# Kernel tuning notes

Measured on AMD Instinct MI355X. Metric: run time of the kernel, lower is better.

The kernel has to match this reference:

```python
import jax, jax.numpy as jnp
import numpy as np

V = 50000; H = 600; HH = 300; L = 100; MAX_LEN = 50; T_IN = 48; T_TGT = 50; EOS = 1


def setup_inputs() -> dict:
    key = jax.random.key(0)
    ks = iter(jax.random.split(key, 40))
    def p(shape, s=0.05):
        return jax.random.normal(next(ks), shape, dtype=jnp.float32) * s
    inp = {}
    inp["emb_enc"] = p((V, H)); inp["emb_dec"] = p((V, H))
    for pre in ["enc", "dec"]:
        for d in ["f", "b"]:
            inp[pre + "_wih_" + d] = p((3 * HH, H))
            inp[pre + "_whh_" + d] = p((3 * HH, HH))
            inp[pre + "_bih_" + d] = p((3 * HH,))
            inp[pre + "_bhh_" + d] = p((3 * HH,))
    inp["w_mean"] = p((L, H)); inp["b_mean"] = p((L,))
    inp["w_logv"] = p((L, H)); inp["b_logv"] = p((L,))
    inp["w_l2h"] = p((H, L)); inp["b_l2h"] = p((H,))
    inp["attn_w"] = p((MAX_LEN, 2 * H)); inp["attn_b"] = p((MAX_LEN,))
    inp["comb_w"] = p((H, 2 * H)); inp["comb_b"] = p((H,))
    inp["out_w"] = p((V, H)); inp["out_b"] = p((V,))
    inp["eps"] = jax.random.normal(next(ks), (MAX_LEN, L), dtype=jnp.float32)
    inp["input_tokens"] = jax.random.randint(next(ks), (T_IN,), 0, V)
    inp["target_tokens"] = jax.random.randint(next(ks), (T_TGT,), 0, V)
    return inp


def _gru_cell(x, h, wih, whh, bih, bhh):
    # PyTorch GRUCell math: r,z,n gates
    gi = wih @ x + bih
    gh = whh @ h + bhh
    ir, iz, inn = jnp.split(gi, 3)
    hr, hz, hn = jnp.split(gh, 3)
    r = jax.nn.sigmoid(ir + hr)
    zg = jax.nn.sigmoid(iz + hz)
    n = jnp.tanh(inn + r * hn)
    return (1.0 - zg) * n + zg * h


def _forward(emb_enc, emb_dec,
             enc_wih_f, enc_whh_f, enc_bih_f, enc_bhh_f,
             enc_wih_b, enc_whh_b, enc_bih_b, enc_bhh_b,
             dec_wih_f, dec_whh_f, dec_bih_f, dec_bhh_f,
             dec_wih_b, dec_whh_b, dec_bih_b, dec_bhh_b,
             w_mean, b_mean, w_logv, b_logv, w_l2h, b_l2h,
             attn_w, attn_b, comb_w, comb_b, out_w, out_b,
             eps, input_tokens, target_tokens):
    # --- encoder: bidirectional GRU fed one token at a time (both dirs see the
    # same forward stream since the original calls the GRU with seq_len=1) ---
    def enc_step(carry, tok):
        hf, hb = carry
        x = emb_enc[tok]
        hf2 = _gru_cell(x, hf, enc_wih_f, enc_whh_f, enc_bih_f, enc_bhh_f)
        hb2 = _gru_cell(x, hb, enc_wih_b, enc_whh_b, enc_bih_b, enc_bhh_b)
        return (hf2, hb2), jnp.concatenate([hf2, hb2])
    h0 = jnp.zeros((HH,), dtype=emb_enc.dtype)
    (hf, hb), enc_out = jax.lax.scan(enc_step, (h0, h0), input_tokens)
    enc_outputs = jnp.zeros((MAX_LEN, H), dtype=emb_enc.dtype).at[:input_tokens.shape[0]].set(enc_out)
    # --- latent ---
    mean = enc_outputs @ w_mean.T + b_mean          # (MAX_LEN, L)
    logv = enc_outputs @ w_logv.T + b_logv          # (MAX_LEN, L)
    z = eps * jnp.exp(0.5 * logv) + mean
    latent_out = z @ w_l2h.T + b_l2h                # (MAX_LEN, H)
    # --- decoder with attention over latent_out (teacher forcing) ---
    dec_in = jnp.concatenate([jnp.array([EOS], dtype=target_tokens.dtype), target_tokens[:-1]])
    def dec_step(carry, tok):
        hf, hb = carry
        emb = emb_dec[tok]                          # (H,) dropout==identity (eval)
        hflat = jnp.concatenate([hf, hb])           # (H,)
        aw = jax.nn.softmax(attn_w @ jnp.concatenate([emb, hflat]) + attn_b)  # (MAX_LEN,)
        applied = aw @ latent_out                   # (H,)
        o = jax.nn.relu(comb_w @ jnp.concatenate([emb, applied]) + comb_b)
        hf2 = _gru_cell(o, hf, dec_wih_f, dec_whh_f, dec_bih_f, dec_bhh_f)
        hb2 = _gru_cell(o, hb, dec_wih_b, dec_whh_b, dec_bih_b, dec_bhh_b)
        logp = jax.nn.log_softmax(out_w @ jnp.concatenate([hf2, hb2]) + out_b)
        return (hf2, hb2), logp
    _, decoded = jax.lax.scan(dec_step, (hf, hb), dec_in)  # (T_TGT, V)
    return decoded, mean, logv


def reference(emb_enc, emb_dec,
              enc_wih_f, enc_whh_f, enc_bih_f, enc_bhh_f,
              enc_wih_b, enc_whh_b, enc_bih_b, enc_bhh_b,
              dec_wih_f, dec_whh_f, dec_bih_f, dec_bhh_f,
              dec_wih_b, dec_whh_b, dec_bih_b, dec_bhh_b,
              w_mean, b_mean, w_logv, b_logv, w_l2h, b_l2h,
              attn_w, attn_b, comb_w, comb_b, out_w, out_b,
              eps, input_tokens, target_tokens):
    return _forward(emb_enc, emb_dec,
                    enc_wih_f, enc_whh_f, enc_bih_f, enc_bhh_f,
                    enc_wih_b, enc_whh_b, enc_bih_b, enc_bhh_b,
                    dec_wih_f, dec_whh_f, dec_bih_f, dec_bhh_f,
                    dec_wih_b, dec_whh_b, dec_bih_b, dec_bhh_b,
                    w_mean, b_mean, w_logv, b_logv, w_l2h, b_l2h,
                    attn_w, attn_b, comb_w, comb_b, out_w, out_b,
                    eps, input_tokens, target_tokens)
```

## Files before the change

### kernel.cpp

```cpp
#include <hip/hip_runtime.h>
#include <math.h>

#define VSZ 50000
#define HD 600
#define HHD 300
#define LATD 100
#define MLEN 50
#define TIN 48
#define TTGT 50
#define NBLK 75
#define NTHR 512
#define NTOT (NBLK*NTHR)
#define ESTR 640
#define SLOT_STRIDE 32
#define SENTU 0x40000000u

typedef __attribute__((ext_vector_type(4))) float f32x4;
typedef __attribute__((ext_vector_type(8))) short s16x8;

__device__ __forceinline__ float sigf(float x){ return 1.0f/(1.0f+__expf(-x)); }

__device__ __forceinline__ void stf(float* p, float v){
    __hip_atomic_store((unsigned int*)p, __float_as_uint(v),
                       __ATOMIC_RELAXED, __HIP_MEMORY_SCOPE_AGENT);
}
__device__ __forceinline__ void stu(float* p, unsigned v){
    __hip_atomic_store((unsigned int*)p, v,
                       __ATOMIC_RELAXED, __HIP_MEMORY_SCOPE_AGENT);
}
__device__ __forceinline__ int ldslot(const int* p){
    return __hip_atomic_load(p, __ATOMIC_RELAXED, __HIP_MEMORY_SCOPE_AGENT);
}
__device__ __forceinline__ void stslot(int* p, int v){
    __hip_atomic_store(p, v, __ATOMIC_RELAXED, __HIP_MEMORY_SCOPE_AGENT);
}

__device__ __forceinline__ f32x4 ld_unc16(const float* p){
    f32x4 r;
    asm volatile("global_load_dwordx4 %0, %1, off sc0 sc1\n\ts_waitcnt vmcnt(0)"
                 : "=v"(r) : "v"(p) : "memory");
    return r;
}
__device__ __forceinline__ f32x4 poll16(const float* p){
    f32x4 r = ld_unc16(p);
    while (__float_as_uint(r[0])==SENTU || __float_as_uint(r[1])==SENTU ||
           __float_as_uint(r[2])==SENTU || __float_as_uint(r[3])==SENTU){
        __builtin_amdgcn_s_sleep(1);
        r = ld_unc16(p);
    }
    return r;
}

__device__ __forceinline__ void redu3(float&a,float&b,float&c){
    #pragma unroll
    for(int off=32;off;off>>=1){
        a+=__shfl_xor(a,off); b+=__shfl_xor(b,off); c+=__shfl_xor(c,off);
    }
}
__device__ __forceinline__ void redu6(float&a,float&b,float&c,float&d,float&e,float&f){
    #pragma unroll
    for(int off=32;off;off>>=1){
        a+=__shfl_xor(a,off); b+=__shfl_xor(b,off); c+=__shfl_xor(c,off);
        d+=__shfl_xor(d,off); e+=__shfl_xor(e,off); f+=__shfl_xor(f,off);
    }
}

__device__ __forceinline__ void gridbar(int* slots, int* flags, int e){
    asm volatile("s_waitcnt vmcnt(0)" ::: "memory");
    __syncthreads();
    const int tid = threadIdx.x;
    if (tid == 0) stslot(&slots[blockIdx.x*SLOT_STRIDE], e);
    if (blockIdx.x == 0){
        if (tid < NBLK){
            while (ldslot(&slots[tid*SLOT_STRIDE]) < e)
                __builtin_amdgcn_s_sleep(1);
        }
        __syncthreads();
        if (tid < NBLK) stslot(&flags[tid*SLOT_STRIDE], e);
    } else {
        if (tid == 0){
            while (ldslot(&flags[blockIdx.x*SLOT_STRIDE]) < e)
                __builtin_amdgcn_s_sleep(1);
        }
    }
    __syncthreads();
}

__global__ void k_init(int* sync_mem){
    int i = blockIdx.x*blockDim.x + threadIdx.x;
    if (i < 2*NBLK*SLOT_STRIDE) sync_mem[i] = 0;
}

__global__ void __launch_bounds__(NTHR) k_seq(
    const float* __restrict__ emb_enc, const float* __restrict__ emb_dec,
    const float* __restrict__ enc_wih_f, const float* __restrict__ enc_whh_f,
    const float* __restrict__ enc_bih_f, const float* __restrict__ enc_bhh_f,
    const float* __restrict__ enc_wih_b, const float* __restrict__ enc_whh_b,
    const float* __restrict__ enc_bih_b, const float* __restrict__ enc_bhh_b,
    const float* __restrict__ dec_wih_f, const float* __restrict__ dec_whh_f,
    const float* __restrict__ dec_bih_f, const float* __restrict__ dec_bhh_f,
    const float* __restrict__ dec_wih_b, const float* __restrict__ dec_whh_b,
    const float* __restrict__ dec_bih_b, const float* __restrict__ dec_bhh_b,
    const float* __restrict__ w_mean, const float* __restrict__ b_mean,
    const float* __restrict__ w_logv, const float* __restrict__ b_logv,
    const float* __restrict__ w_l2h, const float* __restrict__ b_l2h,
    const float* __restrict__ attn_w, const float* __restrict__ attn_b,
    const float* __restrict__ comb_w, const float* __restrict__ comb_b,
    const float* __restrict__ eps, const int* __restrict__ in_toks,
    const int* __restrict__ tgt_toks,
    float* __restrict__ GIf, float* __restrict__ ENCf,
    float* __restrict__ Zf, float* __restrict__ LATf, float* __restrict__ Mf,
    float* __restrict__ APREf, float* __restrict__ CPREf,
    float* __restrict__ HSs, float* __restrict__ HSv,
    float* __restrict__ out_mean, float* __restrict__ out_logv,
    int* slots, int* flags){

    __shared__ float h_lds[ESTR];
    __shared__ float o_lds[ESTR];
    __shared__ float s_lds[64];
    __shared__ float aw_lds[64];
    __shared__ float hv_lds[8];
    __shared__ float big_lds[HD*MLEN];

    const int tid  = threadIdx.x;
    const int lane = tid & 63;
    const int wid  = tid >> 6;
    const int gtid = blockIdx.x*NTHR + tid;
    const int gw   = blockIdx.x*8 + wid;
    const int dir  = gw / HHD;
    const int k    = gw % HHD;
    int ep = 0;

    if (tid < ESTR-HD){ h_lds[HD+tid]=0.f; o_lds[HD+tid]=0.f; }

    for (int idx=gtid; idx<TIN*HD; idx+=NTOT){
        int t=idx/HD, j=idx%HD;
        stu(&ENCf[(long)t*ESTR + j], SENTU);
    }
    for (int idx=gtid; idx<TTGT*HD; idx+=NTOT){
        int t=idx/HD, j=idx%HD;
        stu(&HSs[(long)t*ESTR + j], SENTU);
    }
    for (int idx=gtid; idx<TIN*1800; idx+=NTOT){
        int t=idx/1800, r=idx%1800, d=r/900, j=r%900;
        const float* w  = d ? enc_wih_b : enc_wih_f;
        const float* bi = d ? enc_bih_b : enc_bih_f;
        const float* x  = emb_enc + (long)in_toks[t]*HD;
        const float* wr = w + (long)j*HD;
        float acc = bi[j];
        for (int kk=0;kk<HD;kk+=4){
            float4 wv = *(const float4*)(wr+kk);
            float4 xv = *(const float4*)(x+kk);
            acc = fmaf(wv.x,xv.x,acc); acc = fmaf(wv.y,xv.y,acc);
            acc = fmaf(wv.z,xv.z,acc); acc = fmaf(wv.w,xv.w,acc);
        }
        stf(&GIf[idx], acc);
    }
    for (int idx=gtid; idx<TTGT*MLEN; idx+=NTOT){
        int t=idx/MLEN, a=idx%MLEN;
        int tok = t ? tgt_toks[t-1] : 1;
        const float* x  = emb_dec + (long)tok*HD;
        const float* wr = attn_w + (long)a*1200;
        float acc = attn_b[a];
        for (int kk=0;kk<HD;kk+=4){
            float4 wv = *(const float4*)(wr+kk);
            float4 xv = *(const float4*)(x+kk);
            acc = fmaf(wv.x,xv.x,acc); acc = fmaf(wv.y,xv.y,acc);
            acc = fmaf(wv.z,xv.z,acc); acc = fmaf(wv.w,xv.w,acc);
        }
        stf(&APREf[idx], acc);
    }
    for (int idx=gtid; idx<TTGT*HD; idx+=NTOT){
        int t=idx/HD, j=idx%HD;
        int tok = t ? tgt_toks[t-1] : 1;
        const float* x  = emb_dec + (long)tok*HD;
        const float* wr = comb_w + (long)j*1200;
        float acc = comb_b[j];
        for (int kk=0;kk<HD;kk+=4){
            float4 wv = *(const float4*)(wr+kk);
            float4 xv = *(const float4*)(x+kk);
            acc = fmaf(wv.x,xv.x,acc); acc = fmaf(wv.y,xv.y,acc);
            acc = fmaf(wv.z,xv.z,acc); acc = fmaf(wv.w,xv.w,acc);
        }
        stf(&CPREf[idx], acc);
    }
    gridbar(slots, flags, ++ep);

    {
        const float* whh = dir ? enc_whh_b : enc_whh_f;
        const float* bhh = dir ? enc_bhh_b : enc_bhh_f;
        float wr_[5], wz_[5], wn_[5];
        #pragma unroll
        for (int i=0;i<5;i++){
            int k2 = lane + 64*i;
            bool ok = k2 < HHD;
            wr_[i] = ok ? whh[(long)k*HHD + k2] : 0.f;
            wz_[i] = ok ? whh[(long)(HHD+k)*HHD + k2] : 0.f;
            wn_[i] = ok ? whh[(long)(2*HHD+k)*HHD + k2] : 0.f;
        }
        const float bhr = bhh[k], bhz = bhh[HHD+k], bhn = bhh[2*HHD+k];
        float gr=0, gz=0, gn=0;
        if (lane < TIN){
            const float* g = GIf + (long)lane*1800 + dir*900;
            gr = g[k]; gz = g[HHD+k]; gn = g[2*HHD+k];
        }
        for (int t=0; t<TIN; t++){
            if (t){
                if (tid < HD/4)
                    *(f32x4*)&h_lds[4*tid] = poll16(&ENCf[(long)(t-1)*ESTR + 4*tid]);
            } else {
                h_lds[tid] = 0.f;
                if (tid < HD-NTHR) h_lds[NTHR+tid] = 0.f;
            }
            __syncthreads();
            if (t){
                big_lds[(long)(t-1)*HD + tid] = h_lds[tid];
                if (tid < HD-NTHR) big_lds[(long)(t-1)*HD + NTHR + tid] = h_lds[NTHR+tid];
            }
            float sr=0, sz=0, sn=0;
            #pragma unroll
            for (int i=0;i<5;i++){
                float hv = h_lds[dir*HHD + lane + 64*i];
                sr = fmaf(wr_[i], hv, sr);
                sz = fmaf(wz_[i], hv, sz);
                sn = fmaf(wn_[i], hv, sn);
            }
            redu3(sr, sz, sn);
            float grt=__shfl(gr,t), gzt=__shfl(gz,t), gnt=__shfl(gn,t);
            if (lane==0){
                float r = sigf(grt + sr + bhr);
                float z = sigf(gzt + sz + bhz);
                float n = tanhf(gnt + r*(sn + bhn));
                float hp = h_lds[gw];
                hv_lds[wid] = (1.f-z)*n + z*hp;
            }
            __syncthreads();
            if (tid < 8) stf(&ENCf[(long)t*ESTR + blockIdx.x*8 + tid], hv_lds[tid]);
        }
        if (tid < HD/4)
            *(f32x4*)&h_lds[4*tid] = poll16(&ENCf[(long)(TIN-1)*ESTR + 4*tid]);
        __syncthreads();
        big_lds[(long)(TIN-1)*HD + tid] = h_lds[tid];
        if (tid < HD-NTHR) big_lds[(long)(TIN-1)*HD + NTHR + tid] = h_lds[NTHR+tid];
        big_lds[TIN*HD + tid] = 0.f;
        big_lds[TIN*HD + NTHR + tid] = 0.f;
        if (tid < 2*HD - 2*NTHR) big_lds[TIN*HD + 2*NTHR + tid] = 0.f;
        __syncthreads();
    }

    for (int idx=gtid; idx<MLEN*LATD; idx+=NTOT){
        int i=idx/LATD, l=idx%LATD;
        const float* e = &big_lds[(long)i*HD];
        const float* wmr = w_mean + (long)l*HD;
        float am = b_mean[l];
        for (int kk=0;kk<HD;kk+=4){
            f32x4 wv = *(const f32x4*)(wmr+kk);
            f32x4 ev = *(const f32x4*)(e+kk);
            am = fmaf(wv[0],ev[0],am); am = fmaf(wv[1],ev[1],am);
            am = fmaf(wv[2],ev[2],am); am = fmaf(wv[3],ev[3],am);
        }
        const float* wlr = w_logv + (long)l*HD;
        float al = b_logv[l];
        for (int kk=0;kk<HD;kk+=4){
            f32x4 wv = *(const f32x4*)(wlr+kk);
            f32x4 ev = *(const f32x4*)(e+kk);
            al = fmaf(wv[0],ev[0],al); al = fmaf(wv[1],ev[1],al);
            al = fmaf(wv[2],ev[2],al); al = fmaf(wv[3],ev[3],al);
        }
        out_mean[idx] = am;
        out_logv[idx] = al;
        stf(&Zf[idx], eps[idx]*__expf(0.5f*al) + am);
    }
    gridbar(slots, flags, ++ep);
    for (int idx=gtid; idx<MLEN*HD; idx+=NTOT){
        int i=idx/HD, j=idx%HD;
        const float* zr = Zf + (long)i*LATD;
        const float* wr = w_l2h + (long)j*LATD;
        float acc = b_l2h[j];
        for (int kk=0;kk<LATD;kk+=4){
            float4 wv = *(const float4*)(wr+kk);
            float4 zv = *(const float4*)(zr+kk);
            acc = fmaf(wv.x,zv.x,acc); acc = fmaf(wv.y,zv.y,acc);
            acc = fmaf(wv.z,zv.z,acc); acc = fmaf(wv.w,zv.w,acc);
        }
        stf(&LATf[idx], acc);
    }
    gridbar(slots, flags, ++ep);
    for (int idx=gtid; idx<MLEN*HD; idx+=NTOT){
        int j=idx/MLEN, i=idx%MLEN;
        const float* wr = comb_w + (long)j*1200 + HD;
        const float* lr = LATf + (long)i*HD;
        float acc = 0.f;
        for (int kk=0;kk<HD;kk+=4){
            float4 wv = *(const float4*)(wr+kk);
            float4 lv = *(const float4*)(lr+kk);
            acc = fmaf(wv.x,lv.x,acc); acc = fmaf(wv.y,lv.y,acc);
            acc = fmaf(wv.z,lv.z,acc); acc = fmaf(wv.w,lv.w,acc);
        }
        stf(&Mf[idx], acc);
    }
    gridbar(slots, flags, ++ep);

    {
        for (int idx=tid; idx<HD*MLEN/4; idx+=NTHR)
            *(f32x4*)&big_lds[4*idx] = *(const f32x4*)&Mf[4*idx];

        const float* wih = dir ? dec_wih_b : dec_wih_f;
        const float* bih = dir ? dec_bih_b : dec_bih_f;
        const float* whh = dir ? dec_whh_b : dec_whh_f;
        const float* bhh = dir ? dec_bhh_b : dec_bhh_f;
        float ur[10], uz[10], un[10];
        #pragma unroll
        for (int i=0;i<10;i++){
            int k2 = lane + 64*i;
            bool ok = k2 < HD;
            ur[i] = ok ? wih[(long)k*HD + k2] : 0.f;
            uz[i] = ok ? wih[(long)(HHD+k)*HD + k2] : 0.f;
            un[i] = ok ? wih[(long)(2*HHD+k)*HD + k2] : 0.f;
        }
        float vr[5], vz[5], vn[5];
        #pragma unroll
        for (int i=0;i<5;i++){
            int k2 = lane + 64*i;
            bool ok = k2 < HHD;
            vr[i] = ok ? whh[(long)k*HHD + k2] : 0.f;
            vz[i] = ok ? whh[(long)(HHD+k)*HHD + k2] : 0.f;
            vn[i] = ok ? whh[(long)(2*HHD+k)*HHD + k2] : 0.f;
        }
        const float bir = bih[k], biz = bih[HHD+k], bin_ = bih[2*HHD+k];
        const float bhr = bhh[k], bhz = bhh[HHD+k], bhn = bhh[2*HHD+k];

        for (int t=0; t<TTGT; t++){
            if (t){
                if (tid < HD/4)
                    *(f32x4*)&h_lds[4*tid] = poll16(&HSs[(long)(t-1)*ESTR + 4*tid]);
            }
            float cp0 = CPREf[(long)t*HD + tid];
            float cp1 = (tid < HD-NTHR) ? CPREf[(long)t*HD + NTHR + tid] : 0.f;
            __syncthreads();
            for (int a=wid; a<MLEN; a+=8){
                const float* arow = attn_w + (long)a*1200 + HD;
                float acc = 0.f;
                #pragma unroll
                for (int i=0;i<10;i++){
                    int kk = lane + 64*i;
                    if (kk < HD) acc = fmaf(arow[kk], h_lds[kk], acc);
                }
                #pragma unroll
                for (int off=32;off;off>>=1) acc += __shfl_xor(acc,off);
                if (lane==0) s_lds[a] = acc + APREf[t*MLEN + a];
            }
            __syncthreads();
            if (tid==0){
                float m = -1e30f;
                for (int a=0;a<MLEN;a++) m = fmaxf(m, s_lds[a]);
                float sum = 0.f;
                for (int a=0;a<MLEN;a++){ float e = __expf(s_lds[a]-m); aw_lds[a]=e; sum+=e; }
                float inv = 1.f/sum;
                for (int a=0;a<MLEN;a++) aw_lds[a] *= inv;
            }
            __syncthreads();
            {
                float acc = cp0;
                const float* mr = &big_lds[tid*MLEN];
                #pragma unroll
                for (int i=0;i<MLEN;i++) acc = fmaf(mr[i], aw_lds[i], acc);
                o_lds[tid] = fmaxf(acc, 0.f);
                if (tid < HD-NTHR){
                    float acc2 = cp1;
                    const float* mr2 = &big_lds[(NTHR+tid)*MLEN];
                    #pragma unroll
                    for (int i=0;i<MLEN;i++) acc2 = fmaf(mr2[i], aw_lds[i], acc2);
                    o_lds[NTHR+tid] = fmaxf(acc2, 0.f);
                }
            }
            __syncthreads();
            float ar=0,az=0,an=0, hr=0,hz=0,hn=0;
            #pragma unroll
            for (int i=0;i<10;i++){
                float ov = o_lds[lane + 64*i];
                ar = fmaf(ur[i], ov, ar);
                az = fmaf(uz[i], ov, az);
                an = fmaf(un[i], ov, an);
            }
            #pragma unroll
            for (int i=0;i<5;i++){
                float hv = h_lds[dir*HHD + lane + 64*i];
                hr = fmaf(vr[i], hv, hr);
                hz = fmaf(vz[i], hv, hz);
                hn = fmaf(vn[i], hv, hn);
            }
            redu6(ar,az,an,hr,hz,hn);
            if (lane==0){
                float r = sigf(ar + bir + hr + bhr);
                float zg = sigf(az + biz + hz + bhz);
                float n = tanhf(an + bin_ + r*(hn + bhn));
                hv_lds[wid] = (1.f-zg)*n + zg*h_lds[gw];
            }
            __syncthreads();
            if (tid < 8){
                float hnew = hv_lds[tid];
                stf(&HSs[(long)t*ESTR + blockIdx.x*8 + tid], hnew);
                HSv[(long)t*HD + blockIdx.x*8 + tid] = hnew;
            }
        }
    }
}

__device__ __forceinline__ s16x8 pack8(const float* __restrict__ p){
    s16x8 r;
    #pragma unroll
    for (int i=0;i<8;i++){
        unsigned u = __float_as_uint(p[i]);
        r[i] = (short)((u + 0x7fffu + ((u>>16)&1u)) >> 16);
    }
    return r;
}

__global__ void __launch_bounds__(256) k_vocab(const float* __restrict__ out_w,
        const float* __restrict__ out_b, const float* __restrict__ HS,
        float* __restrict__ logits){
    int lane = threadIdx.x & 63, wid = threadIdx.x >> 6;
    int vbase = blockIdx.x*64 + wid*16;
    int arow  = vbase + (lane & 15);
    int kg    = (lane >> 4) * 8;
    bool aok  = arow < VSZ;
    const float* ap = out_w + (long)(aok ? arow : 0) * HD;
    int t0 = lane & 15;
    f32x4 acc0 = {0,0,0,0}, acc1 = acc0, acc2 = acc0, acc3 = acc0;
    const s16x8 zf = (s16x8)0;

    for (int ks=0; ks<19; ks++){
        int kb = ks*32 + kg;
        bool kok = kb < HD;
        s16x8 a = (aok && kok) ? pack8(ap + kb) : zf;
        s16x8 b0 = kok              ? pack8(HS + (long)(t0     )*HD + kb) : zf;
        s16x8 b1 = kok              ? pack8(HS + (long)(t0 + 16)*HD + kb) : zf;
        s16x8 b2 = kok              ? pack8(HS + (long)(t0 + 32)*HD + kb) : zf;
        s16x8 b3 = (kok && t0 < 2)  ? pack8(HS + (long)(t0 + 48)*HD + kb) : zf;
        acc0 = __builtin_amdgcn_mfma_f32_16x16x32_bf16(a, b0, acc0, 0,0,0);
        acc1 = __builtin_amdgcn_mfma_f32_16x16x32_bf16(a, b1, acc1, 0,0,0);
        acc2 = __builtin_amdgcn_mfma_f32_16x16x32_bf16(a, b2, acc2, 0,0,0);
        acc3 = __builtin_amdgcn_mfma_f32_16x16x32_bf16(a, b3, acc3, 0,0,0);
    }

    int vst = vbase + (lane>>4)*4;
    float bb[4];
    #pragma unroll
    for (int r=0;r<4;r++) bb[r] = (vst+r < VSZ) ? out_b[vst+r] : 0.f;
    #pragma unroll
    for (int f=0; f<4; f++){
        int t = t0 + 16*f;
        if (t >= TTGT) continue;
        const f32x4 acc = f==0?acc0 : f==1?acc1 : f==2?acc2 : acc3;
        float* rowp = logits + (long)t*VSZ;
        #pragma unroll
        for (int r=0;r<4;r++){
            int v = vst + r;
            if (v < VSZ) rowp[v] = acc[r] + bb[r];
        }
    }
}

__global__ void __launch_bounds__(1024) k_lsm(float* __restrict__ logits){
    __shared__ float red[16];
    __shared__ float sm, sl;
    long t = blockIdx.x;
    float* row = logits + t*VSZ;
    int tid = threadIdx.x, lane = tid&63, w = tid>>6;
    float m = -1e30f;
    for (int v=tid; v<VSZ; v+=1024) m = fmaxf(m, row[v]);
    #pragma unroll
    for (int off=32;off;off>>=1) m = fmaxf(m, __shfl_xor(m,off));
    if (lane==0) red[w] = m;
    __syncthreads();
    if (tid==0){ float mm=red[0]; for (int i=1;i<16;i++) mm=fmaxf(mm,red[i]); sm=mm; }
    __syncthreads();
    float mx = sm;
    float s = 0.f;
    for (int v=tid; v<VSZ; v+=1024) s += __expf(row[v]-mx);
    #pragma unroll
    for (int off=32;off;off>>=1) s += __shfl_xor(s,off);
    __syncthreads();
    if (lane==0) red[w] = s;
    __syncthreads();
    if (tid==0){ float ss=0.f; for (int i=0;i<16;i++) ss+=red[i]; sl = logf(ss); }
    __syncthreads();
    float lg = sl;
    for (int v=tid; v<VSZ; v+=1024) row[v] = row[v] - mx - lg;
}

extern "C" void kernel_launch(void* const* d_in, const int* in_sizes, int n_in,
                              void* d_out, int out_size, void* d_ws, size_t ws_size,
                              hipStream_t stream) {
    const float* emb_enc   = (const float*)d_in[0];
    const float* emb_dec   = (const float*)d_in[1];
    const float* enc_wih_f = (const float*)d_in[2];
    const float* enc_whh_f = (const float*)d_in[3];
    const float* enc_bih_f = (const float*)d_in[4];
    const float* enc_bhh_f = (const float*)d_in[5];
    const float* enc_wih_b = (const float*)d_in[6];
    const float* enc_whh_b = (const float*)d_in[7];
    const float* enc_bih_b = (const float*)d_in[8];
    const float* enc_bhh_b = (const float*)d_in[9];
    const float* dec_wih_f = (const float*)d_in[10];
    const float* dec_whh_f = (const float*)d_in[11];
    const float* dec_bih_f = (const float*)d_in[12];
    const float* dec_bhh_f = (const float*)d_in[13];
    const float* dec_wih_b = (const float*)d_in[14];
    const float* dec_whh_b = (const float*)d_in[15];
    const float* dec_bih_b = (const float*)d_in[16];
    const float* dec_bhh_b = (const float*)d_in[17];
    const float* w_mean    = (const float*)d_in[18];
    const float* b_mean    = (const float*)d_in[19];
    const float* w_logv    = (const float*)d_in[20];
    const float* b_logv    = (const float*)d_in[21];
    const float* w_l2h     = (const float*)d_in[22];
    const float* b_l2h     = (const float*)d_in[23];
    const float* attn_w    = (const float*)d_in[24];
    const float* attn_b    = (const float*)d_in[25];
    const float* comb_w    = (const float*)d_in[26];
    const float* comb_b    = (const float*)d_in[27];
    const float* out_w     = (const float*)d_in[28];
    const float* out_b     = (const float*)d_in[29];
    const float* eps       = (const float*)d_in[30];
    const int*   in_toks   = (const int*)d_in[31];
    const int*   tgt_toks  = (const int*)d_in[32];

    float* ws = (float*)d_ws;
    float* GIf   = ws;
    float* ENCf  = ws + 86400;
    float* Zf    = ws + 118400;
    float* LATf  = ws + 123424;
    float* Mf    = ws + 153440;
    float* APREf = ws + 183456;
    float* CPREf = ws + 185984;
    float* HSs   = ws + 216000;
    float* HSv   = ws + 248000;
    int*   slots = (int*)(ws + 278016);
    int*   flags = (int*)(ws + 280416);

    float* dec_out  = (float*)d_out;
    float* out_mean = dec_out + 2500000;
    float* out_logv = dec_out + 2505000;

    k_init<<<(2*NBLK*SLOT_STRIDE + 255)/256, 256, 0, stream>>>((int*)(ws + 278016));

    k_seq<<<NBLK, NTHR, 0, stream>>>(
        emb_enc, emb_dec,
        enc_wih_f, enc_whh_f, enc_bih_f, enc_bhh_f,
        enc_wih_b, enc_whh_b, enc_bih_b, enc_bhh_b,
        dec_wih_f, dec_whh_f, dec_bih_f, dec_bhh_f,
        dec_wih_b, dec_whh_b, dec_bih_b, dec_bhh_b,
        w_mean, b_mean, w_logv, b_logv, w_l2h, b_l2h,
        attn_w, attn_b, comb_w, comb_b,
        eps, in_toks, tgt_toks,
        GIf, ENCf, Zf, LATf, Mf, APREf, CPREf, HSs, HSv,
        out_mean, out_logv, slots, flags);

    k_vocab<<<(VSZ + 63)/64, 256, 0, stream>>>(out_w, out_b, HSv, dec_out);
    k_lsm<<<TTGT, 1024, 0, stream>>>(dec_out);
}
```

Baseline: 850.2 us.

## Shrink persistent recurrent grid to 10 blocks with four hidden units per wave

The persistent sequential kernel drops from 75×512 to 10×1024 threads, and each wave now computes four GRU hidden units whose weights stay in registers. Per-step results are written with uncached 16-byte stores. The embedding and input projections plus sentinel initialisation move to a separate wide pre-kernel, which removes the first grid barrier. Attention weights are also cached in registers for the decoder. Fewer blocks should make the per-step cross-block polling cheaper, at the cost of much higher register pressure and less parallelism per step.

```diff
diff --git a/kernel.cpp b/kernel.cpp
--- a/kernel.cpp
+++ b/kernel.cpp
@@ -8,8 +8,8 @@
 #define MLEN 50
 #define TIN 48
 #define TTGT 50
-#define NBLK 75
-#define NTHR 512
+#define NBLK 10
+#define NTHR 1024
 #define NTOT (NBLK*NTHR)
 #define ESTR 640
 #define SLOT_STRIDE 32
@@ -22,10 +22,6 @@
 
 __device__ __forceinline__ void stf(float* p, float v){
     __hip_atomic_store((unsigned int*)p, __float_as_uint(v),
-                       __ATOMIC_RELAXED, __HIP_MEMORY_SCOPE_AGENT);
-}
-__device__ __forceinline__ void stu(float* p, unsigned v){
-    __hip_atomic_store((unsigned int*)p, v,
                        __ATOMIC_RELAXED, __HIP_MEMORY_SCOPE_AGENT);
 }
 __device__ __forceinline__ int ldslot(const int* p){
@@ -40,6 +36,10 @@
     asm volatile("global_load_dwordx4 %0, %1, off sc0 sc1\n\ts_waitcnt vmcnt(0)"
                  : "=v"(r) : "v"(p) : "memory");
     return r;
+}
+__device__ __forceinline__ void st_unc16(float* p, f32x4 v){
+    asm volatile("global_store_dwordx4 %0, %1, off sc0 sc1"
+                 :: "v"(p), "v"(v) : "memory");
 }
 __device__ __forceinline__ f32x4 poll16(const float* p){
     f32x4 r = ld_unc16(p);
@@ -88,60 +88,26 @@
 
 __global__ void k_init(int* sync_mem){
     int i = blockIdx.x*blockDim.x + threadIdx.x;
-    if (i < 2*NBLK*SLOT_STRIDE) sync_mem[i] = 0;
-}
-
-__global__ void __launch_bounds__(NTHR) k_seq(
+    if (i < 2*64*SLOT_STRIDE) sync_mem[i] = 0;
+}
+
+__global__ void __launch_bounds__(512) k_pre(
     const float* __restrict__ emb_enc, const float* __restrict__ emb_dec,
-    const float* __restrict__ enc_wih_f, const float* __restrict__ enc_whh_f,
-    const float* __restrict__ enc_bih_f, const float* __restrict__ enc_bhh_f,
-    const float* __restrict__ enc_wih_b, const float* __restrict__ enc_whh_b,
-    const float* __restrict__ enc_bih_b, const float* __restrict__ enc_bhh_b,
-    const float* __restrict__ dec_wih_f, const float* __restrict__ dec_whh_f,
-    const float* __restrict__ dec_bih_f, const float* __restrict__ dec_bhh_f,
-    const float* __restrict__ dec_wih_b, const float* __restrict__ dec_whh_b,
-    const float* __restrict__ dec_bih_b, const float* __restrict__ dec_bhh_b,
-    const float* __restrict__ w_mean, const float* __restrict__ b_mean,
-    const float* __restrict__ w_logv, const float* __restrict__ b_logv,
-    const float* __restrict__ w_l2h, const float* __restrict__ b_l2h,
+    const float* __restrict__ enc_wih_f, const float* __restrict__ enc_bih_f,
+    const float* __restrict__ enc_wih_b, const float* __restrict__ enc_bih_b,
     const float* __restrict__ attn_w, const float* __restrict__ attn_b,
     const float* __restrict__ comb_w, const float* __restrict__ comb_b,
-    const float* __restrict__ eps, const int* __restrict__ in_toks,
-    const int* __restrict__ tgt_toks,
-    float* __restrict__ GIf, float* __restrict__ ENCf,
-    float* __restrict__ Zf, float* __restrict__ LATf, float* __restrict__ Mf,
-    float* __restrict__ APREf, float* __restrict__ CPREf,
-    float* __restrict__ HSs, float* __restrict__ HSv,
-    float* __restrict__ out_mean, float* __restrict__ out_logv,
-    int* slots, int* flags){
-
-    __shared__ float h_lds[ESTR];
-    __shared__ float o_lds[ESTR];
-    __shared__ float s_lds[64];
-    __shared__ float aw_lds[64];
-    __shared__ float hv_lds[8];
-    __shared__ float big_lds[HD*MLEN];
-
-    const int tid  = threadIdx.x;
-    const int lane = tid & 63;
-    const int wid  = tid >> 6;
-    const int gtid = blockIdx.x*NTHR + tid;
-    const int gw   = blockIdx.x*8 + wid;
-    const int dir  = gw / HHD;
-    const int k    = gw % HHD;
-    int ep = 0;
-
-    if (tid < ESTR-HD){ h_lds[HD+tid]=0.f; o_lds[HD+tid]=0.f; }
-
-    for (int idx=gtid; idx<TIN*HD; idx+=NTOT){
-        int t=idx/HD, j=idx%HD;
-        stu(&ENCf[(long)t*ESTR + j], SENTU);
-    }
-    for (int idx=gtid; idx<TTGT*HD; idx+=NTOT){
-        int t=idx/HD, j=idx%HD;
-        stu(&HSs[(long)t*ESTR + j], SENTU);
-    }
-    for (int idx=gtid; idx<TIN*1800; idx+=NTOT){
+    const int* __restrict__ in_toks, const int* __restrict__ tgt_toks,
+    float* __restrict__ GIf, float* __restrict__ APREf, float* __restrict__ CPREf,
+    float* __restrict__ ENCf, float* __restrict__ HSs){
+    const int g  = blockIdx.x*512 + threadIdx.x;
+    const int NT = gridDim.x*512;
+    const float SENT = __uint_as_float(SENTU);
+    for (int idx=g; idx<TIN*HD; idx+=NT)
+        ENCf[(long)(idx/HD)*ESTR + idx%HD] = SENT;
+    for (int idx=g; idx<TTGT*HD; idx+=NT)
+        HSs[(long)(idx/HD)*ESTR + idx%HD] = SENT;
+    for (int idx=g; idx<TIN*1800; idx+=NT){
         int t=idx/1800, r=idx%1800, d=r/900, j=r%900;
         const float* w  = d ? enc_wih_b : enc_wih_f;
         const float* bi = d ? enc_bih_b : enc_bih_f;
@@ -154,9 +120,9 @@
             acc = fmaf(wv.x,xv.x,acc); acc = fmaf(wv.y,xv.y,acc);
             acc = fmaf(wv.z,xv.z,acc); acc = fmaf(wv.w,xv.w,acc);
         }
-        stf(&GIf[idx], acc);
-    }
-    for (int idx=gtid; idx<TTGT*MLEN; idx+=NTOT){
+        GIf[idx] = acc;
+    }
+    for (int idx=g; idx<TTGT*MLEN; idx+=NT){
         int t=idx/MLEN, a=idx%MLEN;
         int tok = t ? tgt_toks[t-1] : 1;
         const float* x  = emb_dec + (long)tok*HD;
@@ -168,9 +134,9 @@
             acc = fmaf(wv.x,xv.x,acc); acc = fmaf(wv.y,xv.y,acc);
             acc = fmaf(wv.z,xv.z,acc); acc = fmaf(wv.w,xv.w,acc);
         }
-        stf(&APREf[idx], acc);
-    }
-    for (int idx=gtid; idx<TTGT*HD; idx+=NTOT){
+        APREf[idx] = acc;
+    }
+    for (int idx=g; idx<TTGT*HD; idx+=NT){
         int t=idx/HD, j=idx%HD;
         int tok = t ? tgt_toks[t-1] : 1;
         const float* x  = emb_dec + (long)tok*HD;
@@ -182,69 +148,115 @@
             acc = fmaf(wv.x,xv.x,acc); acc = fmaf(wv.y,xv.y,acc);
             acc = fmaf(wv.z,xv.z,acc); acc = fmaf(wv.w,xv.w,acc);
         }
-        stf(&CPREf[idx], acc);
-    }
-    gridbar(slots, flags, ++ep);
+        CPREf[idx] = acc;
+    }
+}
+
+__global__ void __launch_bounds__(NTHR) k_seq(
+    const float* __restrict__ enc_whh_f, const float* __restrict__ enc_bhh_f,
+    const float* __restrict__ enc_whh_b, const float* __restrict__ enc_bhh_b,
+    const float* __restrict__ dec_wih_f, const float* __restrict__ dec_whh_f,
+    const float* __restrict__ dec_bih_f, const float* __restrict__ dec_bhh_f,
+    const float* __restrict__ dec_wih_b, const float* __restrict__ dec_whh_b,
+    const float* __restrict__ dec_bih_b, const float* __restrict__ dec_bhh_b,
+    const float* __restrict__ w_mean, const float* __restrict__ b_mean,
+    const float* __restrict__ w_logv, const float* __restrict__ b_logv,
+    const float* __restrict__ w_l2h, const float* __restrict__ b_l2h,
+    const float* __restrict__ attn_w, const float* __restrict__ comb_w,
+    const float* __restrict__ eps,
+    const float* __restrict__ GIf, float* __restrict__ ENCf,
+    float* __restrict__ Zf, float* __restrict__ LATf, float* __restrict__ Mf,
+    const float* __restrict__ APREf, const float* __restrict__ CPREf,
+    float* __restrict__ HSs, float* __restrict__ HSv,
+    float* __restrict__ out_mean, float* __restrict__ out_logv,
+    int* slots, int* flags){
+
+    __shared__ float h_lds[ESTR];
+    __shared__ float o_lds[ESTR];
+    __shared__ float s_lds[64];
+    __shared__ float aw_lds[64];
+    __shared__ float big_lds[HD*MLEN];
+
+    const int tid  = threadIdx.x;
+    const int lane = tid & 63;
+    const int wid  = tid >> 6;
+    const int gtid = blockIdx.x*NTHR + tid;
+    const int W    = blockIdx.x*16 + wid;
+    const bool act = W < 150;
+    const int Wc   = act ? W : 0;
+    const int dir  = (Wc*4) / HHD;
+    const int kb   = Wc*4 - dir*HHD;
+    int ep = 0;
+
+    if (tid < ESTR-HD){ h_lds[HD+tid]=0.f; o_lds[HD+tid]=0.f; }
 
     {
         const float* whh = dir ? enc_whh_b : enc_whh_f;
         const float* bhh = dir ? enc_bhh_b : enc_bhh_f;
-        float wr_[5], wz_[5], wn_[5];
+        float wr_[4][5], wz_[4][5], wn_[4][5];
+        float bhr_[4], bhz_[4], bhn_[4];
         #pragma unroll
-        for (int i=0;i<5;i++){
-            int k2 = lane + 64*i;
-            bool ok = k2 < HHD;
-            wr_[i] = ok ? whh[(long)k*HHD + k2] : 0.f;
-            wz_[i] = ok ? whh[(long)(HHD+k)*HHD + k2] : 0.f;
-            wn_[i] = ok ? whh[(long)(2*HHD+k)*HHD + k2] : 0.f;
-        }
-        const float bhr = bhh[k], bhz = bhh[HHD+k], bhn = bhh[2*HHD+k];
-        float gr=0, gz=0, gn=0;
-        if (lane < TIN){
-            const float* g = GIf + (long)lane*1800 + dir*900;
-            gr = g[k]; gz = g[HHD+k]; gn = g[2*HHD+k];
+        for (int q=0;q<4;q++){
+            int kq = kb + q;
+            #pragma unroll
+            for (int i=0;i<5;i++){
+                int k2 = lane + 64*i;
+                bool ok = k2 < HHD;
+                wr_[q][i] = ok ? whh[(long)kq*HHD + k2] : 0.f;
+                wz_[q][i] = ok ? whh[(long)(HHD+kq)*HHD + k2] : 0.f;
+                wn_[q][i] = ok ? whh[(long)(2*HHD+kq)*HHD + k2] : 0.f;
+            }
+            bhr_[q] = bhh[kq]; bhz_[q] = bhh[HHD+kq]; bhn_[q] = bhh[2*HHD+kq];
+        }
+        float gr_[4], gz_[4], gn_[4];
+        #pragma unroll
+        for (int q=0;q<4;q++){
+            if (lane < TIN){
+                const float* g = GIf + (long)lane*1800 + dir*900 + kb + q;
+                gr_[q] = g[0]; gz_[q] = g[HHD]; gn_[q] = g[2*HHD];
+            } else { gr_[q]=0.f; gz_[q]=0.f; gn_[q]=0.f; }
         }
         for (int t=0; t<TIN; t++){
             if (t){
                 if (tid < HD/4)
                     *(f32x4*)&h_lds[4*tid] = poll16(&ENCf[(long)(t-1)*ESTR + 4*tid]);
             } else {
-                h_lds[tid] = 0.f;
-                if (tid < HD-NTHR) h_lds[NTHR+tid] = 0.f;
-            }
-            __syncthreads();
-            if (t){
-                big_lds[(long)(t-1)*HD + tid] = h_lds[tid];
-                if (tid < HD-NTHR) big_lds[(long)(t-1)*HD + NTHR + tid] = h_lds[NTHR+tid];
-            }
-            float sr=0, sz=0, sn=0;
-            #pragma unroll
-            for (int i=0;i<5;i++){
-                float hv = h_lds[dir*HHD + lane + 64*i];
-                sr = fmaf(wr_[i], hv, sr);
-                sz = fmaf(wz_[i], hv, sz);
-                sn = fmaf(wn_[i], hv, sn);
-            }
-            redu3(sr, sz, sn);
-            float grt=__shfl(gr,t), gzt=__shfl(gz,t), gnt=__shfl(gn,t);
-            if (lane==0){
-                float r = sigf(grt + sr + bhr);
-                float z = sigf(gzt + sz + bhz);
-                float n = tanhf(gnt + r*(sn + bhn));
-                float hp = h_lds[gw];
-                hv_lds[wid] = (1.f-z)*n + z*hp;
-            }
-            __syncthreads();
-            if (tid < 8) stf(&ENCf[(long)t*ESTR + blockIdx.x*8 + tid], hv_lds[tid]);
+                if (tid < HD) h_lds[tid] = 0.f;
+            }
+            __syncthreads();
+            if (t && tid < HD) big_lds[(long)(t-1)*HD + tid] = h_lds[tid];
+            float hnew[4];
+            #pragma unroll
+            for (int q=0;q<4;q++){
+                float sr=0, sz=0, sn=0;
+                #pragma unroll
+                for (int i=0;i<5;i++){
+                    float hv = h_lds[dir*HHD + lane + 64*i];
+                    sr = fmaf(wr_[q][i], hv, sr);
+                    sz = fmaf(wz_[q][i], hv, sz);
+                    sn = fmaf(wn_[q][i], hv, sn);
+                }
+                redu3(sr, sz, sn);
+                float grt=__shfl(gr_[q],t), gzt=__shfl(gz_[q],t), gnt=__shfl(gn_[q],t);
+                float r = sigf(grt + sr + bhr_[q]);
+                float z = sigf(gzt + sz + bhz_[q]);
+                float n = tanhf(gnt + r*(sn + bhn_[q]));
+                hnew[q] = (1.f-z)*n + z*h_lds[dir*HHD + kb + q];
+            }
+            if (act && lane==0){
+                f32x4 v = {hnew[0], hnew[1], hnew[2], hnew[3]};
+                st_unc16(&ENCf[(long)t*ESTR + W*4], v);
+            }
+            __syncthreads();
         }
         if (tid < HD/4)
             *(f32x4*)&h_lds[4*tid] = poll16(&ENCf[(long)(TIN-1)*ESTR + 4*tid]);
         __syncthreads();
-        big_lds[(long)(TIN-1)*HD + tid] = h_lds[tid];
-        if (tid < HD-NTHR) big_lds[(long)(TIN-1)*HD + NTHR + tid] = h_lds[NTHR+tid];
-        big_lds[TIN*HD + tid] = 0.f;
-        big_lds[TIN*HD + NTHR + tid] = 0.f;
-        if (tid < 2*HD - 2*NTHR) big_lds[TIN*HD + 2*NTHR + tid] = 0.f;
+        if (tid < HD){
+            big_lds[(long)(TIN-1)*HD + tid] = h_lds[tid];
+            big_lds[(long)TIN*HD + tid] = 0.f;
+            big_lds[(long)(TIN+1)*HD + tid] = 0.f;
+        }
         __syncthreads();
     }
 
@@ -305,50 +317,65 @@
         for (int idx=tid; idx<HD*MLEN/4; idx+=NTHR)
             *(f32x4*)&big_lds[4*idx] = *(const f32x4*)&Mf[4*idx];
 
+        float aw_[4][10];
+        #pragma unroll
+        for (int ai=0;ai<4;ai++){
+            int a = wid + 16*ai;
+            #pragma unroll
+            for (int i=0;i<10;i++){
+                int kk = lane + 64*i;
+                aw_[ai][i] = (a < MLEN && kk < HD) ? attn_w[(long)a*1200 + HD + kk] : 0.f;
+            }
+        }
         const float* wih = dir ? dec_wih_b : dec_wih_f;
         const float* bih = dir ? dec_bih_b : dec_bih_f;
         const float* whh = dir ? dec_whh_b : dec_whh_f;
         const float* bhh = dir ? dec_bhh_b : dec_bhh_f;
-        float ur[10], uz[10], un[10];
+        float ur_[4][10], uz_[4][10], un_[4][10];
+        float vr_[4][5], vz_[4][5], vn_[4][5];
+        float bir_[4], biz_[4], bin_[4], bhr_[4], bhz_[4], bhn_[4];
         #pragma unroll
-        for (int i=0;i<10;i++){
-            int k2 = lane + 64*i;
-            bool ok = k2 < HD;
-            ur[i] = ok ? wih[(long)k*HD + k2] : 0.f;
-            uz[i] = ok ? wih[(long)(HHD+k)*HD + k2] : 0.f;
-            un[i] = ok ? wih[(long)(2*HHD+k)*HD + k2] : 0.f;
-        }
-        float vr[5], vz[5], vn[5];
-        #pragma unroll
-        for (int i=0;i<5;i++){
-            int k2 = lane + 64*i;
-            bool ok = k2 < HHD;
-            vr[i] = ok ? whh[(long)k*HHD + k2] : 0.f;
-            vz[i] = ok ? whh[(long)(HHD+k)*HHD + k2] : 0.f;
-            vn[i] = ok ? whh[(long)(2*HHD+k)*HHD + k2] : 0.f;
-        }
-        const float bir = bih[k], biz = bih[HHD+k], bin_ = bih[2*HHD+k];
-        const float bhr = bhh[k], bhz = bhh[HHD+k], bhn = bhh[2*HHD+k];
+        for (int q=0;q<4;q++){
+            int kq = kb + q;
+            #pragma unroll
+            for (int i=0;i<10;i++){
+                int k2 = lane + 64*i;
+                bool ok = k2 < HD;
+                ur_[q][i] = ok ? wih[(long)kq*HD + k2] : 0.f;
+                uz_[q][i] = ok ? wih[(long)(HHD+kq)*HD + k2] : 0.f;
+                un_[q][i] = ok ? wih[(long)(2*HHD+kq)*HD + k2] : 0.f;
+            }
+            #pragma unroll
+            for (int i=0;i<5;i++){
+                int k2 = lane + 64*i;
+                bool ok = k2 < HHD;
+                vr_[q][i] = ok ? whh[(long)kq*HHD + k2] : 0.f;
+                vz_[q][i] = ok ? whh[(long)(HHD+kq)*HHD + k2] : 0.f;
+                vn_[q][i] = ok ? whh[(long)(2*HHD+kq)*HHD + k2] : 0.f;
+            }
+            bir_[q] = bih[kq]; biz_[q] = bih[HHD+kq]; bin_[q] = bih[2*HHD+kq];
+            bhr_[q] = bhh[kq]; bhz_[q] = bhh[HHD+kq]; bhn_[q] = bhh[2*HHD+kq];
+        }
 
         for (int t=0; t<TTGT; t++){
             if (t){
                 if (tid < HD/4)
                     *(f32x4*)&h_lds[4*tid] = poll16(&HSs[(long)(t-1)*ESTR + 4*tid]);
             }
-            float cp0 = CPREf[(long)t*HD + tid];
-            float cp1 = (tid < HD-NTHR) ? CPREf[(long)t*HD + NTHR + tid] : 0.f;
-            __syncthreads();
-            for (int a=wid; a<MLEN; a+=8){
-                const float* arow = attn_w + (long)a*1200 + HD;
-                float acc = 0.f;
-                #pragma unroll
-                for (int i=0;i<10;i++){
-                    int kk = lane + 64*i;
-                    if (kk < HD) acc = fmaf(arow[kk], h_lds[kk], acc);
+            float cp = (tid < HD) ? CPREf[(long)t*HD + tid] : 0.f;
+            __syncthreads();
+            #pragma unroll
+            for (int ai=0;ai<4;ai++){
+                int a = wid + 16*ai;
+                if (a < MLEN){
+                    float acc = 0.f;
+                    #pragma unroll
+                    for (int i=0;i<10;i++)
+                        acc = fmaf(aw_[ai][i], h_lds[lane + 64*i], acc);
+                    #pragma unroll
+                    for (int off=32;off;off>>=1) acc += __shfl_xor(acc,off);
+                    if (lane==0) s_lds[a] = acc + APREf[t*MLEN + a];
                 }
-                #pragma unroll
-                for (int off=32;off;off>>=1) acc += __shfl_xor(acc,off);
-                if (lane==0) s_lds[a] = acc + APREf[t*MLEN + a];
             }
             __syncthreads();
             if (tid==0){
@@ -360,49 +387,44 @@
                 for (int a=0;a<MLEN;a++) aw_lds[a] *= inv;
             }
             __syncthreads();
-            {
-                float acc = cp0;
+            if (tid < HD){
+                float acc = cp;
                 const float* mr = &big_lds[tid*MLEN];
                 #pragma unroll
                 for (int i=0;i<MLEN;i++) acc = fmaf(mr[i], aw_lds[i], acc);
                 o_lds[tid] = fmaxf(acc, 0.f);
-                if (tid < HD-NTHR){
-                    float acc2 = cp1;
-                    const float* mr2 = &big_lds[(NTHR+tid)*MLEN];
-                    #pragma unroll
-                    for (int i=0;i<MLEN;i++) acc2 = fmaf(mr2[i], aw_lds[i], acc2);
-                    o_lds[NTHR+tid] = fmaxf(acc2, 0.f);
+            }
+            __syncthreads();
+            float hnew[4];
+            #pragma unroll
+            for (int q=0;q<4;q++){
+                float ar=0,az=0,an=0, hr=0,hz=0,hn=0;
+                #pragma unroll
+                for (int i=0;i<10;i++){
+                    float ov = o_lds[lane + 64*i];
+                    ar = fmaf(ur_[q][i], ov, ar);
+                    az = fmaf(uz_[q][i], ov, az);
+                    an = fmaf(un_[q][i], ov, an);
                 }
-            }
-            __syncthreads();
-            float ar=0,az=0,an=0, hr=0,hz=0,hn=0;
-            #pragma unroll
-            for (int i=0;i<10;i++){
-                float ov = o_lds[lane + 64*i];
-                ar = fmaf(ur[i], ov, ar);
-                az = fmaf(uz[i], ov, az);
-                an = fmaf(un[i], ov, an);
-            }
-            #pragma unroll
-            for (int i=0;i<5;i++){
-                float hv = h_lds[dir*HHD + lane + 64*i];
-                hr = fmaf(vr[i], hv, hr);
-                hz = fmaf(vz[i], hv, hz);
-                hn = fmaf(vn[i], hv, hn);
-            }
-            redu6(ar,az,an,hr,hz,hn);
-            if (lane==0){
-                float r = sigf(ar + bir + hr + bhr);
-                float zg = sigf(az + biz + hz + bhz);
-                float n = tanhf(an + bin_ + r*(hn + bhn));
-                hv_lds[wid] = (1.f-zg)*n + zg*h_lds[gw];
-            }
-            __syncthreads();
-            if (tid < 8){
-                float hnew = hv_lds[tid];
-                stf(&HSs[(long)t*ESTR + blockIdx.x*8 + tid], hnew);
-                HSv[(long)t*HD + blockIdx.x*8 + tid] = hnew;
-            }
+                #pragma unroll
+                for (int i=0;i<5;i++){
+                    float hv = h_lds[dir*HHD + lane + 64*i];
+                    hr = fmaf(vr_[q][i], hv, hr);
+                    hz = fmaf(vz_[q][i], hv, hz);
+                    hn = fmaf(vn_[q][i], hv, hn);
+                }
+                redu6(ar,az,an,hr,hz,hn);
+                float r = sigf(ar + bir_[q] + hr + bhr_[q]);
+                float zg = sigf(az + biz_[q] + hz + bhz_[q]);
+                float n = tanhf(an + bin_[q] + r*(hn + bhn_[q]));
+                hnew[q] = (1.f-zg)*n + zg*h_lds[dir*HHD + kb + q];
+            }
+            if (act && lane==0){
+                f32x4 v = {hnew[0], hnew[1], hnew[2], hnew[3]};
+                st_unc16(&HSs[(long)t*ESTR + W*4], v);
+                *(f32x4*)&HSv[(long)t*HD + W*4] = v;
+            }
+            __syncthreads();
         }
     }
 }
@@ -538,23 +560,27 @@
     float* HSs   = ws + 216000;
     float* HSv   = ws + 248000;
     int*   slots = (int*)(ws + 278016);
-    int*   flags = (int*)(ws + 280416);
+    int*   flags = (int*)(ws + 280064);
 
     float* dec_out  = (float*)d_out;
     float* out_mean = dec_out + 2500000;
     float* out_logv = dec_out + 2505000;
 
-    k_init<<<(2*NBLK*SLOT_STRIDE + 255)/256, 256, 0, stream>>>((int*)(ws + 278016));
+    k_init<<<(2*64*SLOT_STRIDE + 255)/256, 256, 0, stream>>>((int*)(ws + 278016));
+
+    k_pre<<<150, 512, 0, stream>>>(
+        emb_enc, emb_dec,
+        enc_wih_f, enc_bih_f, enc_wih_b, enc_bih_b,
+        attn_w, attn_b, comb_w, comb_b,
+        in_toks, tgt_toks,
+        GIf, APREf, CPREf, ENCf, HSs);
 
     k_seq<<<NBLK, NTHR, 0, stream>>>(
-        emb_enc, emb_dec,
-        enc_wih_f, enc_whh_f, enc_bih_f, enc_bhh_f,
-        enc_wih_b, enc_whh_b, enc_bih_b, enc_bhh_b,
+        enc_whh_f, enc_bhh_f, enc_whh_b, enc_bhh_b,
         dec_wih_f, dec_whh_f, dec_bih_f, dec_bhh_f,
         dec_wih_b, dec_whh_b, dec_bih_b, dec_bhh_b,
         w_mean, b_mean, w_logv, b_logv, w_l2h, b_l2h,
-        attn_w, attn_b, comb_w, comb_b,
-        eps, in_toks, tgt_toks,
+        attn_w, comb_w, eps,
         GIf, ENCf, Zf, LATf, Mf, APREf, CPREf, HSs, HSv,
         out_mean, out_logv, slots, flags);
 
```

Result: slower. 2.172 ms (+155.5%).

## Poll only own-direction encoder state per step and cache attention weights in registers

Applied to the files above, without the earlier changes.

In the encoder loop each block now polls only the half of the hidden state its direction needs, rather than the full vector. The other half is gathered once after the loop to fill the encoder outputs buffer. The decoder preloads its attention-weight rows into registers and replaces the single-thread softmax with a wave-level shuffle reduction. Launch bounds are changed to request two blocks per CU. Together these aim to shorten the per-step latency on the serial critical path, at the cost of much higher register pressure from the 70-float awr array plus the existing weight registers, which risks spilling.

```diff
diff --git a/kernel.cpp b/kernel.cpp
--- a/kernel.cpp
+++ b/kernel.cpp
@@ -91,7 +91,7 @@
     if (i < 2*NBLK*SLOT_STRIDE) sync_mem[i] = 0;
 }
 
-__global__ void __launch_bounds__(NTHR) k_seq(
+__global__ void __launch_bounds__(NTHR, 2) k_seq(
     const float* __restrict__ emb_enc, const float* __restrict__ emb_dec,
     const float* __restrict__ enc_wih_f, const float* __restrict__ enc_whh_f,
     const float* __restrict__ enc_bih_f, const float* __restrict__ enc_bhh_f,
@@ -131,7 +131,12 @@
     const int k    = gw % HHD;
     int ep = 0;
 
-    if (tid < ESTR-HD){ h_lds[HD+tid]=0.f; o_lds[HD+tid]=0.f; }
+    const int dlo = (blockIdx.x*8) / HHD, dhi = (blockIdx.x*8 + 7) / HHD;
+    const int clo = (dlo==dhi) ? dlo*75 : 0;
+    const int chi = (dlo==dhi) ? clo+75 : 150;
+    const int flo = 4*clo, fhi = 4*chi;
+
+    for (int j=tid; j<ESTR; j+=NTHR){ h_lds[j]=0.f; o_lds[j]=0.f; }
 
     for (int idx=gtid; idx<TIN*HD; idx+=NTOT){
         int t=idx/HD, j=idx%HD;
@@ -206,16 +211,13 @@
         }
         for (int t=0; t<TIN; t++){
             if (t){
-                if (tid < HD/4)
-                    *(f32x4*)&h_lds[4*tid] = poll16(&ENCf[(long)(t-1)*ESTR + 4*tid]);
-            } else {
-                h_lds[tid] = 0.f;
-                if (tid < HD-NTHR) h_lds[NTHR+tid] = 0.f;
+                if (tid < chi-clo)
+                    *(f32x4*)&h_lds[4*(clo+tid)] = poll16(&ENCf[(long)(t-1)*ESTR + 4*(clo+tid)]);
             }
             __syncthreads();
             if (t){
-                big_lds[(long)(t-1)*HD + tid] = h_lds[tid];
-                if (tid < HD-NTHR) big_lds[(long)(t-1)*HD + NTHR + tid] = h_lds[NTHR+tid];
+                for (int j=flo+tid; j<fhi; j+=NTHR)
+                    big_lds[(long)(t-1)*HD + j] = h_lds[j];
             }
             float sr=0, sz=0, sn=0;
             #pragma unroll
@@ -242,9 +244,18 @@
         __syncthreads();
         big_lds[(long)(TIN-1)*HD + tid] = h_lds[tid];
         if (tid < HD-NTHR) big_lds[(long)(TIN-1)*HD + NTHR + tid] = h_lds[NTHR+tid];
-        big_lds[TIN*HD + tid] = 0.f;
-        big_lds[TIN*HD + NTHR + tid] = 0.f;
-        if (tid < 2*HD - 2*NTHR) big_lds[TIN*HD + 2*NTHR + tid] = 0.f;
+        big_lds[(long)TIN*HD + tid] = 0.f;
+        big_lds[(long)TIN*HD + NTHR + tid] = 0.f;
+        if (tid < 2*HD - 2*NTHR) big_lds[(long)TIN*HD + 2*NTHR + tid] = 0.f;
+        {
+            int compn = 150 - (chi - clo);
+            for (int q=tid; q<47*compn; q+=NTHR){
+                int row = q / compn, c = q % compn;
+                int ch = (c < clo) ? c : (c + (chi - clo));
+                *(f32x4*)&big_lds[(long)row*HD + 4*ch] =
+                    poll16(&ENCf[(long)row*ESTR + 4*ch]);
+            }
+        }
         __syncthreads();
     }
 
@@ -304,6 +315,17 @@
     {
         for (int idx=tid; idx<HD*MLEN/4; idx+=NTHR)
             *(f32x4*)&big_lds[4*idx] = *(const f32x4*)&Mf[4*idx];
+
+        float awr[7][10];
+        #pragma unroll
+        for (int ai=0; ai<7; ai++){
+            int a = wid + 8*ai;
+            #pragma unroll
+            for (int i=0;i<10;i++){
+                int kk = lane + 64*i;
+                awr[ai][i] = (a < MLEN && kk < HD) ? attn_w[(long)a*1200 + HD + kk] : 0.f;
+            }
+        }
 
         const float* wih = dir ? dec_wih_b : dec_wih_f;
         const float* bih = dir ? dec_bih_b : dec_bih_f;
@@ -338,41 +360,39 @@
             float cp0 = CPREf[(long)t*HD + tid];
             float cp1 = (tid < HD-NTHR) ? CPREf[(long)t*HD + NTHR + tid] : 0.f;
             __syncthreads();
-            for (int a=wid; a<MLEN; a+=8){
-                const float* arow = attn_w + (long)a*1200 + HD;
-                float acc = 0.f;
+            #pragma unroll
+            for (int ai=0; ai<7; ai++){
+                int a = wid + 8*ai;
+                if (a < MLEN){
+                    float acc = 0.f;
+                    #pragma unroll
+                    for (int i=0;i<10;i++)
+                        acc = fmaf(awr[ai][i], h_lds[lane + 64*i], acc);
+                    #pragma unroll
+                    for (int off=32;off;off>>=1) acc += __shfl_xor(acc,off);
+                    if (lane==0) s_lds[a] = acc + APREf[t*MLEN + a];
+                }
+            }
+            __syncthreads();
+            if (wid==0){
+                float v = (lane<MLEN) ? s_lds[lane] : -1e30f;
+                float m = v;
                 #pragma unroll
-                for (int i=0;i<10;i++){
-                    int kk = lane + 64*i;
-                    if (kk < HD) acc = fmaf(arow[kk], h_lds[kk], acc);
-                }
+                for (int off=32;off;off>>=1) m = fmaxf(m, __shfl_xor(m,off));
+                float e = (lane<MLEN) ? __expf(v-m) : 0.f;
+                float sum = 0.f;
                 #pragma unroll
-                for (int off=32;off;off>>=1) acc += __shfl_xor(acc,off);
-                if (lane==0) s_lds[a] = acc + APREf[t*MLEN + a];
-            }
-            __syncthreads();
-            if (tid==0){
-                float m = -1e30f;
-                for (int a=0;a<MLEN;a++) m = fmaxf(m, s_lds[a]);
-                float sum = 0.f;
-                for (int a=0;a<MLEN;a++){ float e = __expf(s_lds[a]-m); aw_lds[a]=e; sum+=e; }
+                for (int a=0;a<MLEN;a++) sum += __shfl(e, a);
                 float inv = 1.f/sum;
-                for (int a=0;a<MLEN;a++) aw_lds[a] *= inv;
-            }
-            __syncthreads();
-            {
-                float acc = cp0;
-                const float* mr = &big_lds[tid*MLEN];
+                if (lane<MLEN) aw_lds[lane] = e*inv;
+            }
+            __syncthreads();
+            for (int j=tid; j<HD; j+=NTHR){
+                float acc = (j==tid) ? cp0 : cp1;
+                const float* mr = &big_lds[j*MLEN];
                 #pragma unroll
                 for (int i=0;i<MLEN;i++) acc = fmaf(mr[i], aw_lds[i], acc);
-                o_lds[tid] = fmaxf(acc, 0.f);
-                if (tid < HD-NTHR){
-                    float acc2 = cp1;
-                    const float* mr2 = &big_lds[(NTHR+tid)*MLEN];
-                    #pragma unroll
-                    for (int i=0;i<MLEN;i++) acc2 = fmaf(mr2[i], aw_lds[i], acc2);
-                    o_lds[NTHR+tid] = fmaxf(acc2, 0.f);
-                }
+                o_lds[j] = fmaxf(acc, 0.f);
             }
             __syncthreads();
             float ar=0,az=0,an=0, hr=0,hz=0,hn=0;
```

Result: faster. 782.0 us (-8.0%).
